# Optimization experiments

Measured on AMD Instinct MI355X. Metric: run time of the kernel, lower is better.

Reference implementation:

```python
import jax, jax.numpy as jnp
import numpy as np

N_NODES = 10000
N_EDGES = 160000
HIDDEN = 256
HEADS = 8
LN_EPS = 1e-5


def setup_inputs() -> dict:
    key = jax.random.key(0)
    ks = jax.random.split(key, 8)
    s = 1.0 / np.sqrt(HIDDEN)
    return {
        "node_embeddings": jax.random.normal(ks[0], (1, N_NODES, HIDDEN), jnp.float32),
        "edge_index": jax.random.randint(ks[1], (2, N_EDGES), 0, N_NODES, dtype=jnp.int32),
        "Wq": jax.random.normal(ks[2], (HIDDEN, HIDDEN), jnp.float32) * s,
        "Wk": jax.random.normal(ks[3], (HIDDEN, HIDDEN), jnp.float32) * s,
        "Wv": jax.random.normal(ks[4], (HIDDEN, HIDDEN), jnp.float32) * s,
        "Wo": jax.random.normal(ks[5], (HIDDEN, HIDDEN), jnp.float32) * s,
        "ln_gamma": jnp.ones((HIDDEN,), jnp.float32),
        "ln_beta": jnp.zeros((HIDDEN,), jnp.float32),
    }


def reference(node_embeddings, edge_index, Wq, Wk, Wv, Wo, ln_gamma, ln_beta):
    B, N, Dm = node_embeddings.shape
    H = HEADS
    hd = Dm // H
    scale = 1.0 / np.sqrt(hd)

    def heads(x):  # [B,N,Dm] -> [B,H,N,hd]
        return x.reshape(B, N, H, hd).transpose(0, 2, 1, 3)

    Q = heads(node_embeddings @ Wq)
    K = heads(node_embeddings @ Wk)
    V = heads(node_embeddings @ Wv)

    src, dst = edge_index[0], edge_index[1]
    Qe = Q[:, :, src, :]           # [B,H,E,hd]
    Ke = K[:, :, dst, :]
    Ve = V[:, :, dst, :]

    scores = jnp.einsum('bhed,bhed->bhe', Qe, Ke) * scale   # [B,H,E]
    s_t = scores.transpose(2, 0, 1)                          # [E,B,H]
    smax = jax.ops.segment_max(s_t, src, num_segments=N)    # [N,B,H]
    ex = jnp.exp(s_t - smax[src])                            # [E,B,H]
    denom = jax.ops.segment_sum(ex, src, num_segments=N)    # [N,B,H]
    attn = ex / denom[src]                                   # scatter-softmax weights

    wV = attn[..., None] * Ve.transpose(2, 0, 1, 3)          # [E,B,H,hd]
    agg = jax.ops.segment_sum(wV, src, num_segments=N)      # [N,B,H,hd]
    attn_out = agg.transpose(1, 0, 2, 3).reshape(B, N, Dm)   # [B,N,Dm]

    out = attn_out @ Wo
    x = out + node_embeddings
    mu = jnp.mean(x, axis=-1, keepdims=True)
    var = jnp.mean((x - mu) ** 2, axis=-1, keepdims=True)
    return (x - mu) * jax.lax.rsqrt(var + LN_EPS) * ln_gamma + ln_beta
```

## Files before the change

kernel.cpp:

```cpp
#include <hip/hip_runtime.h>

#define NN 10000
#define NE 160000
#define DM 256
#define CAP 96
#define LN_EPSF 1e-5f
#define SCALEF 0.17677669529663687f

typedef unsigned short u16;
typedef __attribute__((ext_vector_type(4))) u16 u16x4;
typedef __attribute__((ext_vector_type(8))) u16 u16x8;
typedef __attribute__((ext_vector_type(4))) float f32x4;
typedef __attribute__((ext_vector_type(8))) short short8;

__device__ __forceinline__ float b2f(u16 u) { return __uint_as_float(((unsigned)u) << 16); }
__device__ __forceinline__ u16 f2b(float f) {
    unsigned u = __float_as_uint(f);
    return (u16)((u + 0x7fffu + ((u >> 16) & 1u)) >> 16);
}
__device__ __forceinline__ int clampi(int v) { return v < 0 ? 0 : (v >= NN ? NN - 1 : v); }

__global__ void k_fill_zero_f32(float* __restrict__ o, int n) {
    int i = blockIdx.x * 256 + threadIdx.x;
    if (i < n) o[i] = 0.f;
}

__global__ void k_prep(const float* __restrict__ Wq, const float* __restrict__ Wk,
                       const float* __restrict__ Wv, const float* __restrict__ Wo,
                       u16* __restrict__ Wt, int* __restrict__ cnt) {
    int id = blockIdx.x * 256 + threadIdx.x;
    if (id < NN) cnt[id] = 0;
    int m = id >> 16;
    int rc = id & 65535;
    int r = rc >> 8, c = rc & 255;
    const float* W = (m == 0) ? Wq : (m == 1) ? Wk : (m == 2) ? Wv : Wo;
    Wt[m * 65536 + c * 256 + r] = f2b(W[r * 256 + c]);
}

__global__ __launch_bounds__(256) void k_qkv_bucket(const float* __restrict__ X, const u16* __restrict__ Wt,
                                                    u16* __restrict__ Q, u16* __restrict__ KV,
                                                    const int* __restrict__ EI, int* __restrict__ cnt,
                                                    int* __restrict__ buck) {
    constexpr int AS = 40;
    __shared__ u16 At[64 * AS];
    __shared__ u16 Bt[256 * AS];
    if (blockIdx.y == 3) {
        int e = blockIdx.x * 256 + threadIdx.x;
        if (e < NE) {
            int s = clampi(EI[e]);
            int slot = atomicAdd(&cnt[s], 1);
            if (slot < CAP) buck[s * CAP + slot] = clampi(EI[NE + e]);
        }
        return;
    }
    if (blockIdx.x >= 157) return;
    const int t = threadIdx.x;
    const int w = t >> 6, l = t & 63, quad = l >> 4, m16 = l & 15;
    const int mat = blockIdx.y;
    const u16* Wm = Wt + mat * 65536;
    const int node0 = blockIdx.x * 64;
    f32x4 acc[4][4];
#pragma unroll
    for (int i = 0; i < 4; i++)
#pragma unroll
        for (int j = 0; j < 4; j++) acc[i][j] = (f32x4){0.f, 0.f, 0.f, 0.f};
    const int arow = t >> 2, ac8 = (t & 3) * 8;
    for (int k0 = 0; k0 < DM; k0 += 32) {
        u16x8 av = {0, 0, 0, 0, 0, 0, 0, 0};
        int anode = node0 + arow;
        if (anode < NN) {
            const float* xp = X + (size_t)anode * DM + k0 + ac8;
            f32x4 a0 = *(const f32x4*)(xp);
            f32x4 a1 = *(const f32x4*)(xp + 4);
            av[0] = f2b(a0[0]); av[1] = f2b(a0[1]); av[2] = f2b(a0[2]); av[3] = f2b(a0[3]);
            av[4] = f2b(a1[0]); av[5] = f2b(a1[1]); av[6] = f2b(a1[2]); av[7] = f2b(a1[3]);
        }
        *(u16x8*)(At + arow * AS + ac8) = av;
        const u16* bsrc = Wm + t * DM + k0;
        u16x8 b0 = *(const u16x8*)(bsrc);
        u16x8 b1 = *(const u16x8*)(bsrc + 8);
        u16x8 b2 = *(const u16x8*)(bsrc + 16);
        u16x8 b3 = *(const u16x8*)(bsrc + 24);
        u16* bd = Bt + t * AS;
        *(u16x8*)(bd) = b0;
        *(u16x8*)(bd + 8) = b1;
        *(u16x8*)(bd + 16) = b2;
        *(u16x8*)(bd + 24) = b3;
        __syncthreads();
        short8 a[4], b[4];
#pragma unroll
        for (int rt = 0; rt < 4; rt++)
            a[rt] = *(const short8*)(At + (rt * 16 + m16) * AS + quad * 8);
#pragma unroll
        for (int ct = 0; ct < 4; ct++)
            b[ct] = *(const short8*)(Bt + (w * 64 + ct * 16 + m16) * AS + quad * 8);
#pragma unroll
        for (int rt = 0; rt < 4; rt++)
#pragma unroll
            for (int ct = 0; ct < 4; ct++)
                acc[rt][ct] = __builtin_amdgcn_mfma_f32_16x16x32_bf16(a[rt], b[ct], acc[rt][ct], 0, 0, 0);
        __syncthreads();
    }
#pragma unroll
    for (int rt = 0; rt < 4; rt++) {
#pragma unroll
        for (int ct = 0; ct < 4; ct++) {
            int col = w * 64 + ct * 16 + m16;
#pragma unroll
            for (int r = 0; r < 4; r++) {
                int node = node0 + rt * 16 + quad * 4 + r;
                if (node < NN) {
                    u16 v = f2b(acc[rt][ct][r]);
                    if (mat == 0) Q[(size_t)node * DM + col] = v;
                    else KV[(size_t)node * 512 + (col >> 2) * 8 + (col & 3) + ((mat == 2) ? 4 : 0)] = v;
                }
            }
        }
    }
}

#define UPD(mm, ss, AA, kv, p) do {                  \
    float nm_ = fmaxf(mm, p);                        \
    float al_ = __expf(mm - nm_);                    \
    float pe_ = __expf(p - nm_);                     \
    ss = ss * al_ + pe_;                             \
    AA[0] = AA[0] * al_ + pe_ * b2f(kv[4]);          \
    AA[1] = AA[1] * al_ + pe_ * b2f(kv[5]);          \
    AA[2] = AA[2] * al_ + pe_ * b2f(kv[6]);          \
    AA[3] = AA[3] * al_ + pe_ * b2f(kv[7]);          \
    mm = nm_;                                        \
} while (0)

__global__ __launch_bounds__(256) void k_edge(const u16* __restrict__ Q, const u16* __restrict__ KV,
                                              const int* __restrict__ cnt, const int* __restrict__ buck,
                                              u16* __restrict__ attn) {
    const int t = threadIdx.x;
    const int w = t >> 6, l = t & 63;
    const int node = blockIdx.x * 4 + w;
    const int d0 = l * 4;
    int deg = cnt[node];
    if (deg > CAP) deg = CAP;
    const int* bl = buck + node * CAP;
    u16x4 q4 = *(const u16x4*)(Q + (size_t)node * DM + d0);
    float qf0 = b2f(q4[0]) * SCALEF, qf1 = b2f(q4[1]) * SCALEF;
    float qf2 = b2f(q4[2]) * SCALEF, qf3 = b2f(q4[3]) * SCALEF;
    float m0 = -3.0e38f, m1 = -3.0e38f, m2 = -3.0e38f, m3 = -3.0e38f;
    float s0 = 0.f, s1 = 0.f, s2 = 0.f, s3 = 0.f;
    f32x4 A0 = {0.f, 0.f, 0.f, 0.f}, A1 = {0.f, 0.f, 0.f, 0.f};
    f32x4 A2 = {0.f, 0.f, 0.f, 0.f}, A3 = {0.f, 0.f, 0.f, 0.f};
    int i = 0;
    int deg4 = deg & ~3;
    for (; i < deg4; i += 4) {
        int4 e4 = *(const int4*)(bl + i);
        u16x8 kv0 = *(const u16x8*)(KV + (size_t)e4.x * 512 + l * 8);
        u16x8 kv1 = *(const u16x8*)(KV + (size_t)e4.y * 512 + l * 8);
        u16x8 kv2 = *(const u16x8*)(KV + (size_t)e4.z * 512 + l * 8);
        u16x8 kv3 = *(const u16x8*)(KV + (size_t)e4.w * 512 + l * 8);
        float p0 = qf0 * b2f(kv0[0]) + qf1 * b2f(kv0[1]) + qf2 * b2f(kv0[2]) + qf3 * b2f(kv0[3]);
        float p1 = qf0 * b2f(kv1[0]) + qf1 * b2f(kv1[1]) + qf2 * b2f(kv1[2]) + qf3 * b2f(kv1[3]);
        float p2 = qf0 * b2f(kv2[0]) + qf1 * b2f(kv2[1]) + qf2 * b2f(kv2[2]) + qf3 * b2f(kv2[3]);
        float p3 = qf0 * b2f(kv3[0]) + qf1 * b2f(kv3[1]) + qf2 * b2f(kv3[2]) + qf3 * b2f(kv3[3]);
        p0 += __shfl_xor(p0, 1, 64); p1 += __shfl_xor(p1, 1, 64);
        p2 += __shfl_xor(p2, 1, 64); p3 += __shfl_xor(p3, 1, 64);
        p0 += __shfl_xor(p0, 2, 64); p1 += __shfl_xor(p1, 2, 64);
        p2 += __shfl_xor(p2, 2, 64); p3 += __shfl_xor(p3, 2, 64);
        p0 += __shfl_xor(p0, 4, 64); p1 += __shfl_xor(p1, 4, 64);
        p2 += __shfl_xor(p2, 4, 64); p3 += __shfl_xor(p3, 4, 64);
        UPD(m0, s0, A0, kv0, p0);
        UPD(m1, s1, A1, kv1, p1);
        UPD(m2, s2, A2, kv2, p2);
        UPD(m3, s3, A3, kv3, p3);
    }
    for (; i < deg; ++i) {
        int dst = bl[i];
        u16x8 kv = *(const u16x8*)(KV + (size_t)dst * 512 + l * 8);
        float p = qf0 * b2f(kv[0]) + qf1 * b2f(kv[1]) + qf2 * b2f(kv[2]) + qf3 * b2f(kv[3]);
        p += __shfl_xor(p, 1, 64);
        p += __shfl_xor(p, 2, 64);
        p += __shfl_xor(p, 4, 64);
        UPD(m0, s0, A0, kv, p);
    }
    float nm = fmaxf(fmaxf(m0, m1), fmaxf(m2, m3));
    float w0 = __expf(m0 - nm), w1 = __expf(m1 - nm);
    float w2 = __expf(m2 - nm), w3 = __expf(m3 - nm);
    float s = s0 * w0 + s1 * w1 + s2 * w2 + s3 * w3;
    float inv = (s > 0.f) ? 1.f / s : 0.f;
    u16x4 o;
    o[0] = f2b((A0[0] * w0 + A1[0] * w1 + A2[0] * w2 + A3[0] * w3) * inv);
    o[1] = f2b((A0[1] * w0 + A1[1] * w1 + A2[1] * w2 + A3[1] * w3) * inv);
    o[2] = f2b((A0[2] * w0 + A1[2] * w1 + A2[2] * w2 + A3[2] * w3) * inv);
    o[3] = f2b((A0[3] * w0 + A1[3] * w1 + A2[3] * w2 + A3[3] * w3) * inv);
    *(u16x4*)(attn + (size_t)node * DM + d0) = o;
}

__global__ __launch_bounds__(256) void k_gemm_out_ln(const u16* __restrict__ In, const u16* __restrict__ WoT,
                                                     const float* __restrict__ X, const float* __restrict__ g,
                                                     const float* __restrict__ b, float* __restrict__ out) {
    constexpr int AS = 40;
    __shared__ u16 At[64 * AS];
    __shared__ u16 Bt[256 * AS];
    __shared__ float gbuf[256], bbuf[256];
    __shared__ float redS[4][64], redQ[4][64];
    __shared__ float muS[64], rsS[64];
    const int t = threadIdx.x;
    gbuf[t] = g[t];
    bbuf[t] = b[t];
    const int w = t >> 6, l = t & 63, quad = l >> 4, m16 = l & 15;
    const int node0 = blockIdx.x * 64;
    f32x4 acc[4][4];
#pragma unroll
    for (int i = 0; i < 4; i++)
#pragma unroll
        for (int j = 0; j < 4; j++) acc[i][j] = (f32x4){0.f, 0.f, 0.f, 0.f};
    const int arow = t >> 2, ac8 = (t & 3) * 8;
    for (int k0 = 0; k0 < DM; k0 += 32) {
        u16x8 av = {0, 0, 0, 0, 0, 0, 0, 0};
        int anode = node0 + arow;
        if (anode < NN) av = *(const u16x8*)(In + (size_t)anode * DM + k0 + ac8);
        *(u16x8*)(At + arow * AS + ac8) = av;
        const u16* bsrc = WoT + t * DM + k0;
        u16x8 b0 = *(const u16x8*)(bsrc);
        u16x8 b1 = *(const u16x8*)(bsrc + 8);
        u16x8 b2 = *(const u16x8*)(bsrc + 16);
        u16x8 b3 = *(const u16x8*)(bsrc + 24);
        u16* bd = Bt + t * AS;
        *(u16x8*)(bd) = b0;
        *(u16x8*)(bd + 8) = b1;
        *(u16x8*)(bd + 16) = b2;
        *(u16x8*)(bd + 24) = b3;
        __syncthreads();
        short8 a[4], bf[4];
#pragma unroll
        for (int rt = 0; rt < 4; rt++)
            a[rt] = *(const short8*)(At + (rt * 16 + m16) * AS + quad * 8);
#pragma unroll
        for (int ct = 0; ct < 4; ct++)
            bf[ct] = *(const short8*)(Bt + (w * 64 + ct * 16 + m16) * AS + quad * 8);
#pragma unroll
        for (int rt = 0; rt < 4; rt++)
#pragma unroll
            for (int ct = 0; ct < 4; ct++)
                acc[rt][ct] = __builtin_amdgcn_mfma_f32_16x16x32_bf16(a[rt], bf[ct], acc[rt][ct], 0, 0, 0);
        __syncthreads();
    }
#pragma unroll
    for (int rt = 0; rt < 4; rt++)
#pragma unroll
        for (int ct = 0; ct < 4; ct++) {
            int col = w * 64 + ct * 16 + m16;
#pragma unroll
            for (int r = 0; r < 4; r++) {
                int node = node0 + rt * 16 + quad * 4 + r;
                float x = (node < NN) ? X[(size_t)node * DM + col] : 0.f;
                acc[rt][ct][r] += x;
            }
        }
#pragma unroll
    for (int rt = 0; rt < 4; rt++) {
#pragma unroll
        for (int r = 0; r < 4; r++) {
            float p1 = acc[rt][0][r] + acc[rt][1][r] + acc[rt][2][r] + acc[rt][3][r];
            float p2 = acc[rt][0][r] * acc[rt][0][r] + acc[rt][1][r] * acc[rt][1][r] +
                       acc[rt][2][r] * acc[rt][2][r] + acc[rt][3][r] * acc[rt][3][r];
#pragma unroll
            for (int o = 1; o < 16; o <<= 1) {
                p1 += __shfl_xor(p1, o, 64);
                p2 += __shfl_xor(p2, o, 64);
            }
            if (m16 == 0) {
                int row = rt * 16 + quad * 4 + r;
                redS[w][row] = p1;
                redQ[w][row] = p2;
            }
        }
    }
    __syncthreads();
    if (t < 64) {
        float s1t = redS[0][t] + redS[1][t] + redS[2][t] + redS[3][t];
        float s2t = redQ[0][t] + redQ[1][t] + redQ[2][t] + redQ[3][t];
        float mm = s1t * (1.f / DM);
        float var = s2t * (1.f / DM) - mm * mm;
        muS[t] = mm;
        rsS[t] = rsqrtf(var + LN_EPSF);
    }
    __syncthreads();
#pragma unroll
    for (int rt = 0; rt < 4; rt++)
#pragma unroll
        for (int ct = 0; ct < 4; ct++) {
            int col = w * 64 + ct * 16 + m16;
#pragma unroll
            for (int r = 0; r < 4; r++) {
                int row = rt * 16 + quad * 4 + r;
                int node = node0 + row;
                if (node < NN)
                    out[(size_t)node * DM + col] = (acc[rt][ct][r] - muS[row]) * rsS[row] * gbuf[col] + bbuf[col];
            }
        }
}

extern "C" void kernel_launch(void* const* d_in, const int* in_sizes, int n_in,
                              void* d_out, int out_size, void* d_ws, size_t ws_size,
                              hipStream_t stream) {
    (void)in_sizes; (void)n_in;
    const float* X  = (const float*)d_in[0];
    const int*   EI = (const int*)d_in[1];
    const float* Wq = (const float*)d_in[2];
    const float* Wk = (const float*)d_in[3];
    const float* Wv = (const float*)d_in[4];
    const float* Wo = (const float*)d_in[5];
    const float* g  = (const float*)d_in[6];
    const float* be = (const float*)d_in[7];

    const size_t SWT  = (size_t)4 * 65536 * 2;
    const size_t SKV  = (size_t)NN * 512 * 2;
    const size_t SAT  = (size_t)NN * DM * 2;
    const size_t SCNT = (size_t)NN * 4;
    const size_t SBK  = (size_t)NN * CAP * 4;
    const size_t need = SWT + SKV + SAT + SCNT + SBK;
    if (ws_size < need) {
        k_fill_zero_f32<<<(out_size + 255) / 256, 256, 0, stream>>>((float*)d_out, out_size);
        return;
    }
    char* p = (char*)d_ws;
    u16* Wt   = (u16*)p; p += SWT;
    u16* KVb  = (u16*)p; p += SKV;
    u16* attn = (u16*)p; p += SAT;
    int* cnt  = (int*)p; p += SCNT;
    int* buck = (int*)p; p += SBK;
    u16* Qb = (u16*)d_out;

    k_prep<<<1024, 256, 0, stream>>>(Wq, Wk, Wv, Wo, Wt, cnt);
    k_qkv_bucket<<<dim3(625, 4), 256, 0, stream>>>(X, Wt, Qb, KVb, EI, cnt, buck);
    k_edge<<<NN / 4, 256, 0, stream>>>(Qb, KVb, cnt, buck, attn);
    k_gemm_out_ln<<<157, 256, 0, stream>>>(attn, Wt + 3 * 65536, X, g, be, (float*)d_out);
}
```

Measured before the change: 143.7 us.

## Fuse QKV GEMMs per tile, widen edge unroll, halve output GEMM tile

The QKV kernel now loads and converts each 64-node X tile into shared memory once and loops over the three weight matrices, instead of launching a separate block per matrix that each reconverts X. The edge kernel processes eight neighbors per iteration with eight independent online-softmax states to expose more memory-level parallelism. The output GEMM+LayerNorm uses 32-row tiles with the whole A tile staged up front, doubling block count for better occupancy. Q moves from the output buffer to its own workspace region, which needs more workspace and fewer parallel QKV blocks.

```diff
diff --git a/kernel.cpp b/kernel.cpp
--- a/kernel.cpp
+++ b/kernel.cpp
@@ -23,100 +23,6 @@
 __global__ void k_fill_zero_f32(float* __restrict__ o, int n) {
     int i = blockIdx.x * 256 + threadIdx.x;
     if (i < n) o[i] = 0.f;
-}
-
-__global__ void k_prep(const float* __restrict__ Wq, const float* __restrict__ Wk,
-                       const float* __restrict__ Wv, const float* __restrict__ Wo,
-                       u16* __restrict__ Wt, int* __restrict__ cnt) {
-    int id = blockIdx.x * 256 + threadIdx.x;
-    if (id < NN) cnt[id] = 0;
-    int m = id >> 16;
-    int rc = id & 65535;
-    int r = rc >> 8, c = rc & 255;
-    const float* W = (m == 0) ? Wq : (m == 1) ? Wk : (m == 2) ? Wv : Wo;
-    Wt[m * 65536 + c * 256 + r] = f2b(W[r * 256 + c]);
-}
-
-__global__ __launch_bounds__(256) void k_qkv_bucket(const float* __restrict__ X, const u16* __restrict__ Wt,
-                                                    u16* __restrict__ Q, u16* __restrict__ KV,
-                                                    const int* __restrict__ EI, int* __restrict__ cnt,
-                                                    int* __restrict__ buck) {
-    constexpr int AS = 40;
-    __shared__ u16 At[64 * AS];
-    __shared__ u16 Bt[256 * AS];
-    if (blockIdx.y == 3) {
-        int e = blockIdx.x * 256 + threadIdx.x;
-        if (e < NE) {
-            int s = clampi(EI[e]);
-            int slot = atomicAdd(&cnt[s], 1);
-            if (slot < CAP) buck[s * CAP + slot] = clampi(EI[NE + e]);
-        }
-        return;
-    }
-    if (blockIdx.x >= 157) return;
-    const int t = threadIdx.x;
-    const int w = t >> 6, l = t & 63, quad = l >> 4, m16 = l & 15;
-    const int mat = blockIdx.y;
-    const u16* Wm = Wt + mat * 65536;
-    const int node0 = blockIdx.x * 64;
-    f32x4 acc[4][4];
-#pragma unroll
-    for (int i = 0; i < 4; i++)
-#pragma unroll
-        for (int j = 0; j < 4; j++) acc[i][j] = (f32x4){0.f, 0.f, 0.f, 0.f};
-    const int arow = t >> 2, ac8 = (t & 3) * 8;
-    for (int k0 = 0; k0 < DM; k0 += 32) {
-        u16x8 av = {0, 0, 0, 0, 0, 0, 0, 0};
-        int anode = node0 + arow;
-        if (anode < NN) {
-            const float* xp = X + (size_t)anode * DM + k0 + ac8;
-            f32x4 a0 = *(const f32x4*)(xp);
-            f32x4 a1 = *(const f32x4*)(xp + 4);
-            av[0] = f2b(a0[0]); av[1] = f2b(a0[1]); av[2] = f2b(a0[2]); av[3] = f2b(a0[3]);
-            av[4] = f2b(a1[0]); av[5] = f2b(a1[1]); av[6] = f2b(a1[2]); av[7] = f2b(a1[3]);
-        }
-        *(u16x8*)(At + arow * AS + ac8) = av;
-        const u16* bsrc = Wm + t * DM + k0;
-        u16x8 b0 = *(const u16x8*)(bsrc);
-        u16x8 b1 = *(const u16x8*)(bsrc + 8);
-        u16x8 b2 = *(const u16x8*)(bsrc + 16);
-        u16x8 b3 = *(const u16x8*)(bsrc + 24);
-        u16* bd = Bt + t * AS;
-        *(u16x8*)(bd) = b0;
-        *(u16x8*)(bd + 8) = b1;
-        *(u16x8*)(bd + 16) = b2;
-        *(u16x8*)(bd + 24) = b3;
-        __syncthreads();
-        short8 a[4], b[4];
-#pragma unroll
-        for (int rt = 0; rt < 4; rt++)
-            a[rt] = *(const short8*)(At + (rt * 16 + m16) * AS + quad * 8);
-#pragma unroll
-        for (int ct = 0; ct < 4; ct++)
-            b[ct] = *(const short8*)(Bt + (w * 64 + ct * 16 + m16) * AS + quad * 8);
-#pragma unroll
-        for (int rt = 0; rt < 4; rt++)
-#pragma unroll
-            for (int ct = 0; ct < 4; ct++)
-                acc[rt][ct] = __builtin_amdgcn_mfma_f32_16x16x32_bf16(a[rt], b[ct], acc[rt][ct], 0, 0, 0);
-        __syncthreads();
-    }
-#pragma unroll
-    for (int rt = 0; rt < 4; rt++) {
-#pragma unroll
-        for (int ct = 0; ct < 4; ct++) {
-            int col = w * 64 + ct * 16 + m16;
-#pragma unroll
-            for (int r = 0; r < 4; r++) {
-                int node = node0 + rt * 16 + quad * 4 + r;
-                if (node < NN) {
-                    u16 v = f2b(acc[rt][ct][r]);
-                    if (mat == 0) Q[(size_t)node * DM + col] = v;
-                    else KV[(size_t)node * 512 + (col >> 2) * 8 + (col & 3) + ((mat == 2) ? 4 : 0)] = v;
-                }
-            }
-        }
-    }
 }
 
 #define UPD(mm, ss, AA, kv, p) do {                  \
@@ -130,6 +36,106 @@
     AA[3] = AA[3] * al_ + pe_ * b2f(kv[7]);          \
     mm = nm_;                                        \
 } while (0)
+
+__global__ void k_prep(const float* __restrict__ Wq, const float* __restrict__ Wk,
+                       const float* __restrict__ Wv, const float* __restrict__ Wo,
+                       u16* __restrict__ Wt, int* __restrict__ cnt) {
+    int id = blockIdx.x * 256 + threadIdx.x;
+    if (id < NN) cnt[id] = 0;
+    int m = id >> 16;
+    int rc = id & 65535;
+    int r = rc >> 8, c = rc & 255;
+    const float* W = (m == 0) ? Wq : (m == 1) ? Wk : (m == 2) ? Wv : Wo;
+    Wt[m * 65536 + c * 256 + r] = f2b(W[r * 256 + c]);
+}
+
+__global__ __launch_bounds__(256) void k_qkv_bucket(const float* __restrict__ X, const u16* __restrict__ Wt,
+                                                    u16* __restrict__ Q, u16* __restrict__ KV,
+                                                    const int* __restrict__ EI, int* __restrict__ cnt,
+                                                    int* __restrict__ buck) {
+    constexpr int BS = 40;
+    constexpr int ASF = 264;
+    __shared__ u16 At[64 * ASF];
+    __shared__ u16 Bt[256 * BS];
+    if (blockIdx.y == 1) {
+        int e = blockIdx.x * 256 + threadIdx.x;
+        if (e < NE) {
+            int s = clampi(EI[e]);
+            int slot = atomicAdd(&cnt[s], 1);
+            if (slot < CAP) buck[s * CAP + slot] = clampi(EI[NE + e]);
+        }
+        return;
+    }
+    if (blockIdx.x >= 157) return;
+    const int t = threadIdx.x;
+    const int w = t >> 6, l = t & 63, quad = l >> 4, m16 = l & 15;
+    const int node0 = blockIdx.x * 64;
+    const int arow = t >> 2, ac8 = (t & 3) * 8;
+    const int anode = node0 + arow;
+#pragma unroll
+    for (int k0 = 0; k0 < DM; k0 += 32) {
+        u16x8 av = {0, 0, 0, 0, 0, 0, 0, 0};
+        if (anode < NN) {
+            const float* xp = X + (size_t)anode * DM + k0 + ac8;
+            f32x4 a0 = *(const f32x4*)(xp);
+            f32x4 a1 = *(const f32x4*)(xp + 4);
+            av[0] = f2b(a0[0]); av[1] = f2b(a0[1]); av[2] = f2b(a0[2]); av[3] = f2b(a0[3]);
+            av[4] = f2b(a1[0]); av[5] = f2b(a1[1]); av[6] = f2b(a1[2]); av[7] = f2b(a1[3]);
+        }
+        *(u16x8*)(At + arow * ASF + k0 + ac8) = av;
+    }
+    __syncthreads();
+    for (int mat = 0; mat < 3; mat++) {
+        const u16* Wm = Wt + mat * 65536;
+        f32x4 acc[4][4];
+#pragma unroll
+        for (int i = 0; i < 4; i++)
+#pragma unroll
+            for (int j = 0; j < 4; j++) acc[i][j] = (f32x4){0.f, 0.f, 0.f, 0.f};
+        for (int k0 = 0; k0 < DM; k0 += 32) {
+            const u16* bsrc = Wm + t * DM + k0;
+            u16x8 b0 = *(const u16x8*)(bsrc);
+            u16x8 b1 = *(const u16x8*)(bsrc + 8);
+            u16x8 b2 = *(const u16x8*)(bsrc + 16);
+            u16x8 b3 = *(const u16x8*)(bsrc + 24);
+            u16* bd = Bt + t * BS;
+            *(u16x8*)(bd) = b0;
+            *(u16x8*)(bd + 8) = b1;
+            *(u16x8*)(bd + 16) = b2;
+            *(u16x8*)(bd + 24) = b3;
+            __syncthreads();
+            short8 a[4], b[4];
+#pragma unroll
+            for (int rt = 0; rt < 4; rt++)
+                a[rt] = *(const short8*)(At + (rt * 16 + m16) * ASF + k0 + quad * 8);
+#pragma unroll
+            for (int ct = 0; ct < 4; ct++)
+                b[ct] = *(const short8*)(Bt + (w * 64 + ct * 16 + m16) * BS + quad * 8);
+#pragma unroll
+            for (int rt = 0; rt < 4; rt++)
+#pragma unroll
+                for (int ct = 0; ct < 4; ct++)
+                    acc[rt][ct] = __builtin_amdgcn_mfma_f32_16x16x32_bf16(a[rt], b[ct], acc[rt][ct], 0, 0, 0);
+            __syncthreads();
+        }
+#pragma unroll
+        for (int rt = 0; rt < 4; rt++) {
+#pragma unroll
+            for (int ct = 0; ct < 4; ct++) {
+                int col = w * 64 + ct * 16 + m16;
+#pragma unroll
+                for (int r = 0; r < 4; r++) {
+                    int node = node0 + rt * 16 + quad * 4 + r;
+                    if (node < NN) {
+                        u16 v = f2b(acc[rt][ct][r]);
+                        if (mat == 0) Q[(size_t)node * DM + col] = v;
+                        else KV[(size_t)node * 512 + (col >> 2) * 8 + (col & 3) + ((mat == 2) ? 4 : 0)] = v;
+                    }
+                }
+            }
+        }
+    }
+}
 
 __global__ __launch_bounds__(256) void k_edge(const u16* __restrict__ Q, const u16* __restrict__ KV,
                                               const int* __restrict__ cnt, const int* __restrict__ buck,
@@ -144,32 +150,36 @@
     u16x4 q4 = *(const u16x4*)(Q + (size_t)node * DM + d0);
     float qf0 = b2f(q4[0]) * SCALEF, qf1 = b2f(q4[1]) * SCALEF;
     float qf2 = b2f(q4[2]) * SCALEF, qf3 = b2f(q4[3]) * SCALEF;
-    float m0 = -3.0e38f, m1 = -3.0e38f, m2 = -3.0e38f, m3 = -3.0e38f;
-    float s0 = 0.f, s1 = 0.f, s2 = 0.f, s3 = 0.f;
-    f32x4 A0 = {0.f, 0.f, 0.f, 0.f}, A1 = {0.f, 0.f, 0.f, 0.f};
-    f32x4 A2 = {0.f, 0.f, 0.f, 0.f}, A3 = {0.f, 0.f, 0.f, 0.f};
+    float mm[8], ss[8];
+    f32x4 AA[8];
+#pragma unroll
+    for (int j = 0; j < 8; j++) {
+        mm[j] = -3.0e38f;
+        ss[j] = 0.f;
+        AA[j] = (f32x4){0.f, 0.f, 0.f, 0.f};
+    }
     int i = 0;
-    int deg4 = deg & ~3;
-    for (; i < deg4; i += 4) {
-        int4 e4 = *(const int4*)(bl + i);
-        u16x8 kv0 = *(const u16x8*)(KV + (size_t)e4.x * 512 + l * 8);
-        u16x8 kv1 = *(const u16x8*)(KV + (size_t)e4.y * 512 + l * 8);
-        u16x8 kv2 = *(const u16x8*)(KV + (size_t)e4.z * 512 + l * 8);
-        u16x8 kv3 = *(const u16x8*)(KV + (size_t)e4.w * 512 + l * 8);
-        float p0 = qf0 * b2f(kv0[0]) + qf1 * b2f(kv0[1]) + qf2 * b2f(kv0[2]) + qf3 * b2f(kv0[3]);
-        float p1 = qf0 * b2f(kv1[0]) + qf1 * b2f(kv1[1]) + qf2 * b2f(kv1[2]) + qf3 * b2f(kv1[3]);
-        float p2 = qf0 * b2f(kv2[0]) + qf1 * b2f(kv2[1]) + qf2 * b2f(kv2[2]) + qf3 * b2f(kv2[3]);
-        float p3 = qf0 * b2f(kv3[0]) + qf1 * b2f(kv3[1]) + qf2 * b2f(kv3[2]) + qf3 * b2f(kv3[3]);
-        p0 += __shfl_xor(p0, 1, 64); p1 += __shfl_xor(p1, 1, 64);
-        p2 += __shfl_xor(p2, 1, 64); p3 += __shfl_xor(p3, 1, 64);
-        p0 += __shfl_xor(p0, 2, 64); p1 += __shfl_xor(p1, 2, 64);
-        p2 += __shfl_xor(p2, 2, 64); p3 += __shfl_xor(p3, 2, 64);
-        p0 += __shfl_xor(p0, 4, 64); p1 += __shfl_xor(p1, 4, 64);
-        p2 += __shfl_xor(p2, 4, 64); p3 += __shfl_xor(p3, 4, 64);
-        UPD(m0, s0, A0, kv0, p0);
-        UPD(m1, s1, A1, kv1, p1);
-        UPD(m2, s2, A2, kv2, p2);
-        UPD(m3, s3, A3, kv3, p3);
+    int deg8 = deg & ~7;
+    for (; i < deg8; i += 8) {
+        int4 ea = *(const int4*)(bl + i);
+        int4 eb = *(const int4*)(bl + i + 4);
+        int dst[8] = {ea.x, ea.y, ea.z, ea.w, eb.x, eb.y, eb.z, eb.w};
+        u16x8 kv[8];
+#pragma unroll
+        for (int j = 0; j < 8; j++)
+            kv[j] = *(const u16x8*)(KV + (size_t)dst[j] * 512 + l * 8);
+        float p[8];
+#pragma unroll
+        for (int j = 0; j < 8; j++)
+            p[j] = qf0 * b2f(kv[j][0]) + qf1 * b2f(kv[j][1]) + qf2 * b2f(kv[j][2]) + qf3 * b2f(kv[j][3]);
+#pragma unroll
+        for (int j = 0; j < 8; j++) p[j] += __shfl_xor(p[j], 1, 64);
+#pragma unroll
+        for (int j = 0; j < 8; j++) p[j] += __shfl_xor(p[j], 2, 64);
+#pragma unroll
+        for (int j = 0; j < 8; j++) p[j] += __shfl_xor(p[j], 4, 64);
+#pragma unroll
+        for (int j = 0; j < 8; j++) UPD(mm[j], ss[j], AA[j], kv[j], p[j]);
     }
     for (; i < deg; ++i) {
         int dst = bl[i];
@@ -178,73 +188,88 @@
         p += __shfl_xor(p, 1, 64);
         p += __shfl_xor(p, 2, 64);
         p += __shfl_xor(p, 4, 64);
-        UPD(m0, s0, A0, kv, p);
-    }
-    float nm = fmaxf(fmaxf(m0, m1), fmaxf(m2, m3));
-    float w0 = __expf(m0 - nm), w1 = __expf(m1 - nm);
-    float w2 = __expf(m2 - nm), w3 = __expf(m3 - nm);
-    float s = s0 * w0 + s1 * w1 + s2 * w2 + s3 * w3;
-    float inv = (s > 0.f) ? 1.f / s : 0.f;
+        UPD(mm[0], ss[0], AA[0], kv, p);
+    }
+    float nm = mm[0];
+#pragma unroll
+    for (int j = 1; j < 8; j++) nm = fmaxf(nm, mm[j]);
+    float S = 0.f, O0 = 0.f, O1 = 0.f, O2 = 0.f, O3 = 0.f;
+#pragma unroll
+    for (int j = 0; j < 8; j++) {
+        float wj = __expf(mm[j] - nm);
+        S += ss[j] * wj;
+        O0 += AA[j][0] * wj;
+        O1 += AA[j][1] * wj;
+        O2 += AA[j][2] * wj;
+        O3 += AA[j][3] * wj;
+    }
+    float inv = (S > 0.f) ? 1.f / S : 0.f;
     u16x4 o;
-    o[0] = f2b((A0[0] * w0 + A1[0] * w1 + A2[0] * w2 + A3[0] * w3) * inv);
-    o[1] = f2b((A0[1] * w0 + A1[1] * w1 + A2[1] * w2 + A3[1] * w3) * inv);
-    o[2] = f2b((A0[2] * w0 + A1[2] * w1 + A2[2] * w2 + A3[2] * w3) * inv);
-    o[3] = f2b((A0[3] * w0 + A1[3] * w1 + A2[3] * w2 + A3[3] * w3) * inv);
+    o[0] = f2b(O0 * inv);
+    o[1] = f2b(O1 * inv);
+    o[2] = f2b(O2 * inv);
+    o[3] = f2b(O3 * inv);
     *(u16x4*)(attn + (size_t)node * DM + d0) = o;
 }
 
 __global__ __launch_bounds__(256) void k_gemm_out_ln(const u16* __restrict__ In, const u16* __restrict__ WoT,
                                                      const float* __restrict__ X, const float* __restrict__ g,
                                                      const float* __restrict__ b, float* __restrict__ out) {
-    constexpr int AS = 40;
-    __shared__ u16 At[64 * AS];
-    __shared__ u16 Bt[256 * AS];
+    constexpr int BS = 40;
+    constexpr int ALS = 264;
+    __shared__ u16 AtL[32 * ALS];
+    __shared__ u16 Bt[256 * BS];
     __shared__ float gbuf[256], bbuf[256];
-    __shared__ float redS[4][64], redQ[4][64];
-    __shared__ float muS[64], rsS[64];
+    __shared__ float redS[4][32], redQ[4][32], muS[32], rsS[32];
     const int t = threadIdx.x;
     gbuf[t] = g[t];
     bbuf[t] = b[t];
     const int w = t >> 6, l = t & 63, quad = l >> 4, m16 = l & 15;
-    const int node0 = blockIdx.x * 64;
-    f32x4 acc[4][4];
-#pragma unroll
-    for (int i = 0; i < 4; i++)
+    const int node0 = blockIdx.x * 32;
+    {
+        const int arow = t >> 3, ac32 = (t & 7) * 32;
+        const int anode = node0 + arow;
+#pragma unroll
+        for (int j = 0; j < 4; j++) {
+            u16x8 av = {0, 0, 0, 0, 0, 0, 0, 0};
+            if (anode < NN) av = *(const u16x8*)(In + (size_t)anode * DM + ac32 + j * 8);
+            *(u16x8*)(AtL + arow * ALS + ac32 + j * 8) = av;
+        }
+    }
+    f32x4 acc[2][4];
+#pragma unroll
+    for (int i = 0; i < 2; i++)
 #pragma unroll
         for (int j = 0; j < 4; j++) acc[i][j] = (f32x4){0.f, 0.f, 0.f, 0.f};
-    const int arow = t >> 2, ac8 = (t & 3) * 8;
+    __syncthreads();
     for (int k0 = 0; k0 < DM; k0 += 32) {
-        u16x8 av = {0, 0, 0, 0, 0, 0, 0, 0};
-        int anode = node0 + arow;
-        if (anode < NN) av = *(const u16x8*)(In + (size_t)anode * DM + k0 + ac8);
-        *(u16x8*)(At + arow * AS + ac8) = av;
         const u16* bsrc = WoT + t * DM + k0;
         u16x8 b0 = *(const u16x8*)(bsrc);
         u16x8 b1 = *(const u16x8*)(bsrc + 8);
         u16x8 b2 = *(const u16x8*)(bsrc + 16);
         u16x8 b3 = *(const u16x8*)(bsrc + 24);
-        u16* bd = Bt + t * AS;
+        u16* bd = Bt + t * BS;
         *(u16x8*)(bd) = b0;
         *(u16x8*)(bd + 8) = b1;
         *(u16x8*)(bd + 16) = b2;
         *(u16x8*)(bd + 24) = b3;
         __syncthreads();
-        short8 a[4], bf[4];
-#pragma unroll
-        for (int rt = 0; rt < 4; rt++)
-            a[rt] = *(const short8*)(At + (rt * 16 + m16) * AS + quad * 8);
+        short8 a[2], bf[4];
+#pragma unroll
+        for (int rt = 0; rt < 2; rt++)
+            a[rt] = *(const short8*)(AtL + (rt * 16 + m16) * ALS + k0 + quad * 8);
 #pragma unroll
         for (int ct = 0; ct < 4; ct++)
-            bf[ct] = *(const short8*)(Bt + (w * 64 + ct * 16 + m16) * AS + quad * 8);
-#pragma unroll
-        for (int rt = 0; rt < 4; rt++)
+            bf[ct] = *(const short8*)(Bt + (w * 64 + ct * 16 + m16) * BS + quad * 8);
+#pragma unroll
+        for (int rt = 0; rt < 2; rt++)
 #pragma unroll
             for (int ct = 0; ct < 4; ct++)
                 acc[rt][ct] = __builtin_amdgcn_mfma_f32_16x16x32_bf16(a[rt], bf[ct], acc[rt][ct], 0, 0, 0);
         __syncthreads();
     }
 #pragma unroll
-    for (int rt = 0; rt < 4; rt++)
+    for (int rt = 0; rt < 2; rt++)
 #pragma unroll
         for (int ct = 0; ct < 4; ct++) {
             int col = w * 64 + ct * 16 + m16;
@@ -256,7 +281,7 @@
             }
         }
 #pragma unroll
-    for (int rt = 0; rt < 4; rt++) {
+    for (int rt = 0; rt < 2; rt++) {
 #pragma unroll
         for (int r = 0; r < 4; r++) {
             float p1 = acc[rt][0][r] + acc[rt][1][r] + acc[rt][2][r] + acc[rt][3][r];
@@ -275,7 +300,7 @@
         }
     }
     __syncthreads();
-    if (t < 64) {
+    if (t < 32) {
         float s1t = redS[0][t] + redS[1][t] + redS[2][t] + redS[3][t];
         float s2t = redQ[0][t] + redQ[1][t] + redQ[2][t] + redQ[3][t];
         float mm = s1t * (1.f / DM);
@@ -285,7 +310,7 @@
     }
     __syncthreads();
 #pragma unroll
-    for (int rt = 0; rt < 4; rt++)
+    for (int rt = 0; rt < 2; rt++)
 #pragma unroll
         for (int ct = 0; ct < 4; ct++) {
             int col = w * 64 + ct * 16 + m16;
@@ -314,10 +339,11 @@
 
     const size_t SWT  = (size_t)4 * 65536 * 2;
     const size_t SKV  = (size_t)NN * 512 * 2;
-    const size_t SAT  = (size_t)NN * DM * 2;
     const size_t SCNT = (size_t)NN * 4;
     const size_t SBK  = (size_t)NN * CAP * 4;
-    const size_t need = SWT + SKV + SAT + SCNT + SBK;
+    const size_t SQB  = (size_t)NN * DM * 2;
+    const size_t SAT  = (size_t)NN * DM * 2;
+    const size_t need = SWT + SKV + SCNT + SBK + SQB + SAT;
     if (ws_size < need) {
         k_fill_zero_f32<<<(out_size + 255) / 256, 256, 0, stream>>>((float*)d_out, out_size);
         return;
@@ -325,13 +351,13 @@
     char* p = (char*)d_ws;
     u16* Wt   = (u16*)p; p += SWT;
     u16* KVb  = (u16*)p; p += SKV;
-    u16* attn = (u16*)p; p += SAT;
     int* cnt  = (int*)p; p += SCNT;
     int* buck = (int*)p; p += SBK;
-    u16* Qb = (u16*)d_out;
+    u16* Qb   = (u16*)p; p += SQB;
+    u16* attn = (u16*)p; p += SAT;
 
     k_prep<<<1024, 256, 0, stream>>>(Wq, Wk, Wv, Wo, Wt, cnt);
-    k_qkv_bucket<<<dim3(625, 4), 256, 0, stream>>>(X, Wt, Qb, KVb, EI, cnt, buck);
+    k_qkv_bucket<<<dim3(625, 2), 256, 0, stream>>>(X, Wt, Qb, KVb, EI, cnt, buck);
     k_edge<<<NN / 4, 256, 0, stream>>>(Qb, KVb, cnt, buck, attn);
-    k_gemm_out_ln<<<157, 256, 0, stream>>>(attn, Wt + 3 * 65536, X, g, be, (float*)d_out);
-}
+    k_gemm_out_ln<<<313, 256, 0, stream>>>(attn, Wt + 3 * 65536, X, g, be, (float*)d_out);
+}
```

Result: slower. 152.7 us (+6.3%).
